# Kernel tuning notes

Hardware: AMD Instinct MI355X
Metric: run time of the kernel (lower is better)

The kernel has to match this reference:

```python
import jax, jax.numpy as jnp
import numpy as np

B, S, D_MODEL, D_FF = 8, 1024, 512, 2048
NCAT, NSUB, TOPK = 8, 8, 2
E = NCAT * NSUB            # 64 experts
CAP = 1024


def setup_inputs() -> dict:
    key = jax.random.key(0)
    ks = jax.random.split(key, 6)
    hidden = jax.random.normal(ks[0], (B, S, D_MODEL), jnp.float32)
    cat_indices = jax.random.randint(ks[1], (B, S, TOPK), 0, NCAT)
    sub_indices = jax.random.randint(ks[2], (B, S, TOPK), 0, NSUB)
    weights = jax.random.uniform(ks[3], (B, S, TOPK), jnp.float32)
    # Stacked per-expert MLP params (Expert = Linear -> GELU -> Linear, dropout off in eval)
    W1 = jax.random.normal(ks[4], (E, D_MODEL, D_FF), jnp.float32) / np.sqrt(D_MODEL).astype(np.float32)
    b1 = jnp.zeros((E, D_FF), jnp.float32)
    W2 = jax.random.normal(ks[5], (E, D_FF, D_MODEL), jnp.float32) / np.sqrt(D_FF).astype(np.float32)
    b2 = jnp.zeros((E, D_MODEL), jnp.float32)
    return dict(hidden=hidden, cat_indices=cat_indices, sub_indices=sub_indices,
                weights=weights, W1=W1, b1=b1, W2=W2, b2=b2)


def _moe_forward(hidden, cat_indices, sub_indices, weights, W1, b1, W2, b2):
    Bq, Sq, d = hidden.shape
    K = cat_indices.shape[-1]
    T = Bq * Sq            # tokens
    A = T * K              # (token, k) routing assignments
    x = hidden.reshape(T, d)
    eid = (cat_indices * NSUB + sub_indices).reshape(A).astype(jnp.int32)  # flat expert id
    wf = weights.reshape(A)
    tok = jnp.arange(A, dtype=jnp.int32) // K  # token index per assignment

    # position of each assignment within its expert's capacity buffer
    oh = jax.nn.one_hot(eid, E, dtype=jnp.int32)                     # [A, E]
    pos = jnp.take_along_axis(jnp.cumsum(oh, axis=0) - 1,
                              eid[:, None].astype(jnp.int32), axis=1)[:, 0]
    valid = (pos < CAP).astype(hidden.dtype)

    # dispatch: gather tokens into [E, CAP, d] buffer (overflow dropped; CAP sized to avoid it)
    buf = jnp.zeros((E, CAP, d), hidden.dtype).at[eid, pos].set(x[tok], mode='drop')

    # grouped expert MLP: Linear -> GELU -> Linear
    h = jax.nn.gelu(jnp.einsum('ecd,edf->ecf', buf, W1) + b1[:, None, :], approximate=False)
    yb = jnp.einsum('ecf,efd->ecd', h, W2) + b2[:, None, :]          # [E, CAP, d]

    # combine: gather each assignment's expert output, weight it, scatter-add over tokens
    pc = jnp.minimum(pos, CAP - 1)
    ya = yb[eid, pc] * (wf * valid)[:, None]                          # [A, d]
    out = jnp.zeros((T, d), hidden.dtype).at[tok].add(ya)
    return out.reshape(Bq, Sq, d)


def reference(hidden, cat_indices, sub_indices, weights, W1, b1, W2, b2):
    return _moe_forward(hidden, cat_indices, sub_indices, weights, W1, b1, W2, b2)
```

## Files before the change

### kernel.cpp

```cpp
#include <hip/hip_runtime.h>
#include <hip/hip_bf16.h>
#include <cstdint>
#include <cstddef>

#define TOKENS 8192
#define ASSIGN 16384
#define DM     512
#define DFF    2048
#define NEXP   64
#define NSUB_  8
#define CAP2   512
#define BK     64
#define BMT    256

typedef __bf16 bf16;
typedef __bf16 bf16x4 __attribute__((ext_vector_type(4)));
typedef __bf16 bf16x8 __attribute__((ext_vector_type(8)));
typedef float  f32x4  __attribute__((ext_vector_type(4)));

__global__ void k_zero(int* __restrict__ count) { count[threadIdx.x] = 0; }

__global__ void k_route(const int* __restrict__ cat, const int* __restrict__ sub,
                        int* __restrict__ count, int* __restrict__ slot_of) {
    int a = blockIdx.x * 256 + threadIdx.x;
    if (a >= ASSIGN) return;
    int e = cat[a] * NSUB_ + sub[a];
    int s = atomicAdd(&count[e], 1);
    slot_of[a] = (s < CAP2) ? (e * CAP2 + s) : -1;
}

__global__ void k_gather(const float* __restrict__ hidden, const int* __restrict__ slot_of,
                         bf16* __restrict__ xg) {
    int a = blockIdx.x * 4 + (threadIdx.x >> 6);
    int t = threadIdx.x & 63;
    int r = slot_of[a];
    if (r < 0) return;
    int tok = a >> 1;
    const f32x4* src = (const f32x4*)(hidden + (size_t)tok * DM);
    f32x4 v0 = src[t * 2], v1 = src[t * 2 + 1];
    bf16x8 o;
    o[0] = (bf16)v0[0]; o[1] = (bf16)v0[1]; o[2] = (bf16)v0[2]; o[3] = (bf16)v0[3];
    o[4] = (bf16)v1[0]; o[5] = (bf16)v1[1]; o[6] = (bf16)v1[2]; o[7] = (bf16)v1[3];
    *(bf16x8*)(xg + (size_t)r * DM + t * 8) = o;
}

__device__ inline float gelu_tanh(float x) {
    float s2 = 1.5957691216057308f * x * (1.0f + 0.044715f * x * x);
    float z = __expf(-fabsf(s2));
    float sig = 1.0f / (1.0f + z);
    return (s2 >= 0.0f) ? x * sig : x * (1.0f - sig);
}

__device__ inline void gload_lds16(const void* g, void* l) {
    __builtin_amdgcn_global_load_lds((const __attribute__((address_space(1))) void*)g,
                                     (__attribute__((address_space(3))) void*)l, 16, 0, 0);
}

template <bool GELU>
__global__ __launch_bounds__(512, 4)
void k_gemm(const bf16* __restrict__ A, const float* __restrict__ W,
            const float* __restrict__ bias, bf16* __restrict__ C,
            const int* __restrict__ count, int N, int K, int ntn) {
    __shared__ __align__(16) char As[2][BMT * 128];
    __shared__ __align__(16) char Bs[128 * 128];

    int nwg = gridDim.x;
    int lg = (int)(blockIdx.x & 7) * (nwg >> 3) + (int)(blockIdx.x >> 3);
    int e = lg / (2 * ntn);
    int rem = lg - e * 2 * ntn;
    int ntile = rem >> 1, mtile = rem & 1;

    int mc = count[e]; if (mc > CAP2) mc = CAP2;
    if (mtile * BMT >= mc) return;
    int tid = threadIdx.x, wave = tid >> 6, lane = tid & 63;
    int wm = wave >> 1, wn = wave & 1;

    const char*  Ag = (const char*)(A + (size_t)(e * CAP2 + mtile * BMT) * K);
    const float* Wg = W + (size_t)e * K * N + (size_t)ntile * 128;

    int kq = ((lane >> 3) & 7) | ((wave & 1) << 3);
    int nq = (lane & 7) | (((wave >> 1) & 3) << 3);

    f32x4 br[4];
    auto issueB = [&](int kt) {
        const float* p = Wg + (size_t)(kt * BK + kq * 4) * N + nq * 4;
        br[0] = *(const f32x4*)(p);
        br[1] = *(const f32x4*)(p + N);
        br[2] = *(const f32x4*)(p + 2 * (size_t)N);
        br[3] = *(const f32x4*)(p + 3 * (size_t)N);
    };
    auto writeB = [&]() {
#pragma unroll
        for (int c = 0; c < 4; c++) {
            int n = nq * 4 + c;
            bf16x4 v;
#pragma unroll
            for (int j = 0; j < 4; j++) v[j] = (bf16)br[j][c];
            *(bf16x4*)(Bs + n * 128 + ((kq * 8) ^ ((n & 7) << 4))) = v;
        }
    };
    auto issueA = [&](int kt, char* dst) {
#pragma unroll
        for (int i = 0; i < 4; i++) {
            int chunk = i * 8 + wave;
            int d = chunk * 1024 + lane * 16;
            int row = d >> 7;
            int col = (d & 127) ^ ((row & 7) << 4);
            gload_lds16(Ag + (size_t)row * (2 * K) + (size_t)kt * 128 + col,
                        dst + chunk * 1024);
        }
    };

    f32x4 acc[4][4];
#pragma unroll
    for (int i = 0; i < 4; i++)
#pragma unroll
        for (int j = 0; j < 4; j++) acc[i][j] = f32x4{0.f, 0.f, 0.f, 0.f};

    int nK = K >> 6;
    issueB(0);
    issueA(0, As[0]);
    asm volatile("s_waitcnt vmcnt(0)" ::: "memory");
    __builtin_amdgcn_sched_barrier(0);

    for (int kt = 0; kt < nK; kt++) {
        int c = kt & 1, n = c ^ 1;
        writeB();
        if (kt + 1 < nK) {
            issueB(kt + 1);
            issueA(kt + 1, As[n]);
        }
        asm volatile("s_waitcnt lgkmcnt(0)" ::: "memory");
        __builtin_amdgcn_s_barrier();
        __builtin_amdgcn_sched_barrier(0);
#pragma unroll
        for (int ks = 0; ks < 2; ks++) {
            bf16x8 af[4], bfv[4];
#pragma unroll
            for (int mi = 0; mi < 4; mi++) {
                int row = wm * 64 + mi * 16 + (lane & 15);
                af[mi] = *(const bf16x8*)(As[c] + row * 128 +
                         ((ks * 64 + (lane >> 4) * 16) ^ ((row & 7) << 4)));
            }
#pragma unroll
            for (int ni = 0; ni < 4; ni++) {
                int nn = wn * 64 + ni * 16 + (lane & 15);
                bfv[ni] = *(const bf16x8*)(Bs + nn * 128 +
                          ((ks * 64 + (lane >> 4) * 16) ^ ((nn & 7) << 4)));
            }
#pragma unroll
            for (int mi = 0; mi < 4; mi++)
#pragma unroll
                for (int ni = 0; ni < 4; ni++)
                    acc[mi][ni] = __builtin_amdgcn_mfma_f32_16x16x32_bf16(
                        af[mi], bfv[ni], acc[mi][ni], 0, 0, 0);
        }
        __builtin_amdgcn_sched_barrier(0);
        asm volatile("s_waitcnt vmcnt(0)" ::: "memory");
        __builtin_amdgcn_s_barrier();
        __builtin_amdgcn_sched_barrier(0);
    }

#pragma unroll
    for (int mi = 0; mi < 4; mi++) {
        int rowb = wm * 64 + mi * 16 + ((lane >> 4) << 2);
#pragma unroll
        for (int ni = 0; ni < 4; ni++) {
            int col = ntile * 128 + wn * 64 + ni * 16 + (lane & 15);
            float bv = bias[e * N + col];
#pragma unroll
            for (int r = 0; r < 4; r++) {
                float v = acc[mi][ni][r] + bv;
                if (GELU) v = gelu_tanh(v);
                int grow = e * CAP2 + mtile * BMT + rowb + r;
                C[(size_t)grow * N + col] = (bf16)v;
            }
        }
    }
}

__global__ void k_combine(const float* __restrict__ wts, const int* __restrict__ slot_of,
                          const bf16* __restrict__ y, float* __restrict__ out) {
    int tok = blockIdx.x * 4 + (threadIdx.x >> 6);
    int t = threadIdx.x & 63;
    float acc[8] = {0, 0, 0, 0, 0, 0, 0, 0};
#pragma unroll
    for (int k = 0; k < 2; k++) {
        int a = tok * 2 + k;
        int r = slot_of[a];
        if (r >= 0) {
            float w = wts[a];
            bf16x8 v = *(const bf16x8*)(y + (size_t)r * DM + t * 8);
#pragma unroll
            for (int j = 0; j < 8; j++) acc[j] += w * (float)v[j];
        }
    }
    f32x4* o = (f32x4*)(out + (size_t)tok * DM + t * 8);
    o[0] = f32x4{acc[0], acc[1], acc[2], acc[3]};
    o[1] = f32x4{acc[4], acc[5], acc[6], acc[7]};
}

extern "C" void kernel_launch(void* const* d_in, const int* in_sizes, int n_in,
                              void* d_out, int out_size, void* d_ws, size_t ws_size,
                              hipStream_t stream) {
    const float* hidden = (const float*)d_in[0];
    const int*   cat    = (const int*)d_in[1];
    const int*   sub    = (const int*)d_in[2];
    const float* wts    = (const float*)d_in[3];
    const float* W1     = (const float*)d_in[4];
    const float* b1     = (const float*)d_in[5];
    const float* W2     = (const float*)d_in[6];
    const float* b2     = (const float*)d_in[7];
    float* out = (float*)d_out;

    char* ws = (char*)d_ws;
    size_t off = 0;
    bf16* hbuf = (bf16*)(ws + off); off += (size_t)NEXP * CAP2 * DFF * 2;
    bf16* xg   = (bf16*)(ws + off); off += (size_t)NEXP * CAP2 * DM * 2;
    bf16* y    = xg;
    int* count   = (int*)(ws + off); off += 256;
    int* slot_of = (int*)(ws + off); off += (size_t)ASSIGN * 4;

    k_zero<<<1, 64, 0, stream>>>(count);
    k_route<<<ASSIGN / 256, 256, 0, stream>>>(cat, sub, count, slot_of);
    k_gather<<<ASSIGN / 4, 256, 0, stream>>>(hidden, slot_of, xg);

    k_gemm<true><<<dim3(NEXP * 16 * 2), 512, 0, stream>>>(
        xg, W1, b1, hbuf, count, DFF, DM, 16);

    k_gemm<false><<<dim3(NEXP * 4 * 2), 512, 0, stream>>>(
        hbuf, W2, b2, y, count, DM, DFF, 4);

    k_combine<<<TOKENS / 4, 256, 0, stream>>>(wts, slot_of, y, out);
}
```

Before: 314.9 us.

## Deepen GEMM prefetch pipeline to three A stages and shrink M-tile

The grouped GEMM now uses 128-row M tiles with 256-thread blocks, so twice as many blocks cover the same work. A is triple-buffered and B double-buffered in LDS, and the prefetch distance is two K-steps. Partial vmcnt waits replace the full drain, so global loads overlap the MFMA work. The cost is that each W tile is now loaded and converted to bf16 by twice as many blocks, which adds global traffic and conversion work.

Result: slower. 378.3 us (+20.1%).

```diff
diff --git a/kernel.cpp b/kernel.cpp
--- a/kernel.cpp
+++ b/kernel.cpp
@@ -11,7 +11,7 @@
 #define NSUB_  8
 #define CAP2   512
 #define BK     64
-#define BMT    256
+#define BMT    128
 
 typedef __bf16 bf16;
 typedef __bf16 bf16x4 __attribute__((ext_vector_type(4)));
@@ -57,18 +57,18 @@
 }
 
 template <bool GELU>
-__global__ __launch_bounds__(512, 4)
+__global__ __launch_bounds__(256, 2)
 void k_gemm(const bf16* __restrict__ A, const float* __restrict__ W,
             const float* __restrict__ bias, bf16* __restrict__ C,
             const int* __restrict__ count, int N, int K, int ntn) {
-    __shared__ __align__(16) char As[2][BMT * 128];
-    __shared__ __align__(16) char Bs[128 * 128];
+    __shared__ __align__(16) char As[3][BMT * 128];
+    __shared__ __align__(16) char Bs[2][128 * 128];
 
     int nwg = gridDim.x;
     int lg = (int)(blockIdx.x & 7) * (nwg >> 3) + (int)(blockIdx.x >> 3);
-    int e = lg / (2 * ntn);
-    int rem = lg - e * 2 * ntn;
-    int ntile = rem >> 1, mtile = rem & 1;
+    int e = lg / (4 * ntn);
+    int rem = lg - e * 4 * ntn;
+    int ntile = rem >> 2, mtile = rem & 3;
 
     int mc = count[e]; if (mc > CAP2) mc = CAP2;
     if (mtile * BMT >= mc) return;
@@ -79,30 +79,37 @@
     const float* Wg = W + (size_t)e * K * N + (size_t)ntile * 128;
 
     int kq = ((lane >> 3) & 7) | ((wave & 1) << 3);
-    int nq = (lane & 7) | (((wave >> 1) & 3) << 3);
-
-    f32x4 br[4];
+
+    f32x4 br[2][4];
     auto issueB = [&](int kt) {
-        const float* p = Wg + (size_t)(kt * BK + kq * 4) * N + nq * 4;
-        br[0] = *(const f32x4*)(p);
-        br[1] = *(const f32x4*)(p + N);
-        br[2] = *(const f32x4*)(p + 2 * (size_t)N);
-        br[3] = *(const f32x4*)(p + 3 * (size_t)N);
+#pragma unroll
+        for (int s = 0; s < 2; s++) {
+            int nq = (lane & 7) + 8 * (((wave >> 1) & 1) + 2 * s);
+            const float* p = Wg + (size_t)(kt * BK + kq * 4) * N + nq * 4;
+            br[s][0] = *(const f32x4*)(p);
+            br[s][1] = *(const f32x4*)(p + N);
+            br[s][2] = *(const f32x4*)(p + 2 * (size_t)N);
+            br[s][3] = *(const f32x4*)(p + 3 * (size_t)N);
+        }
     };
-    auto writeB = [&]() {
-#pragma unroll
-        for (int c = 0; c < 4; c++) {
-            int n = nq * 4 + c;
-            bf16x4 v;
-#pragma unroll
-            for (int j = 0; j < 4; j++) v[j] = (bf16)br[j][c];
-            *(bf16x4*)(Bs + n * 128 + ((kq * 8) ^ ((n & 7) << 4))) = v;
+    auto writeB = [&](char* dst) {
+#pragma unroll
+        for (int s = 0; s < 2; s++) {
+            int nq = (lane & 7) + 8 * (((wave >> 1) & 1) + 2 * s);
+#pragma unroll
+            for (int c = 0; c < 4; c++) {
+                int n = nq * 4 + c;
+                bf16x4 v;
+#pragma unroll
+                for (int j = 0; j < 4; j++) v[j] = (bf16)br[s][j][c];
+                *(bf16x4*)(dst + n * 128 + ((kq * 8) ^ ((n & 7) << 4))) = v;
+            }
         }
     };
     auto issueA = [&](int kt, char* dst) {
 #pragma unroll
         for (int i = 0; i < 4; i++) {
-            int chunk = i * 8 + wave;
+            int chunk = i * 4 + wave;
             int d = chunk * 1024 + lane * 16;
             int row = d >> 7;
             int col = (d & 127) ^ ((row & 7) << 4);
@@ -120,18 +127,21 @@
     int nK = K >> 6;
     issueB(0);
     issueA(0, As[0]);
-    asm volatile("s_waitcnt vmcnt(0)" ::: "memory");
     __builtin_amdgcn_sched_barrier(0);
+    writeB(Bs[0]);
+    issueB(1 < nK ? 1 : 0);
+    issueA(1 < nK ? 1 : 0, As[1]);
+    __builtin_amdgcn_sched_barrier(0);
+    asm volatile("s_waitcnt vmcnt(12)" ::: "memory");
+    asm volatile("s_waitcnt lgkmcnt(0)" ::: "memory");
+    __builtin_amdgcn_s_barrier();
+    __builtin_amdgcn_sched_barrier(0);
 
     for (int kt = 0; kt < nK; kt++) {
-        int c = kt & 1, n = c ^ 1;
-        writeB();
-        if (kt + 1 < nK) {
-            issueB(kt + 1);
-            issueA(kt + 1, As[n]);
-        }
-        asm volatile("s_waitcnt lgkmcnt(0)" ::: "memory");
-        __builtin_amdgcn_s_barrier();
+        int pf = (kt + 2 < nK) ? kt + 2 : nK - 1;
+        writeB(Bs[(kt + 1) & 1]);
+        issueB(pf);
+        issueA(pf, As[(kt + 2) % 3]);
         __builtin_amdgcn_sched_barrier(0);
 #pragma unroll
         for (int ks = 0; ks < 2; ks++) {
@@ -139,13 +149,13 @@
 #pragma unroll
             for (int mi = 0; mi < 4; mi++) {
                 int row = wm * 64 + mi * 16 + (lane & 15);
-                af[mi] = *(const bf16x8*)(As[c] + row * 128 +
+                af[mi] = *(const bf16x8*)(As[kt % 3] + row * 128 +
                          ((ks * 64 + (lane >> 4) * 16) ^ ((row & 7) << 4)));
             }
 #pragma unroll
             for (int ni = 0; ni < 4; ni++) {
                 int nn = wn * 64 + ni * 16 + (lane & 15);
-                bfv[ni] = *(const bf16x8*)(Bs + nn * 128 +
+                bfv[ni] = *(const bf16x8*)(Bs[kt & 1] + nn * 128 +
                           ((ks * 64 + (lane >> 4) * 16) ^ ((nn & 7) << 4)));
             }
 #pragma unroll
@@ -156,7 +166,8 @@
                         af[mi], bfv[ni], acc[mi][ni], 0, 0, 0);
         }
         __builtin_amdgcn_sched_barrier(0);
-        asm volatile("s_waitcnt vmcnt(0)" ::: "memory");
+        asm volatile("s_waitcnt vmcnt(12)" ::: "memory");
+        asm volatile("s_waitcnt lgkmcnt(0)" ::: "memory");
         __builtin_amdgcn_s_barrier();
         __builtin_amdgcn_sched_barrier(0);
     }
@@ -225,10 +236,10 @@
     k_route<<<ASSIGN / 256, 256, 0, stream>>>(cat, sub, count, slot_of);
     k_gather<<<ASSIGN / 4, 256, 0, stream>>>(hidden, slot_of, xg);
 
-    k_gemm<true><<<dim3(NEXP * 16 * 2), 512, 0, stream>>>(
+    k_gemm<true><<<dim3(NEXP * 16 * 4), 256, 0, stream>>>(
         xg, W1, b1, hbuf, count, DFF, DM, 16);
 
-    k_gemm<false><<<dim3(NEXP * 4 * 2), 512, 0, stream>>>(
+    k_gemm<false><<<dim3(NEXP * 4 * 4), 256, 0, stream>>>(
         hbuf, W2, b2, y, count, DM, DFF, 4);
 
     k_combine<<<TOKENS / 4, 256, 0, stream>>>(wts, slot_of, y, out);
```
